# Kernel tuning notes

Hardware: AMD Instinct MI355X
Metric: run time of the kernel (lower is better)

The kernel has to match this reference:

```python
import jax, jax.numpy as jnp
import numpy as np

INNER_DIM = 1024

def setup_inputs() -> dict:
    key = jax.random.key(0)
    ks = jax.random.split(key, 6)
    b, n, d = 4, 4096, 1024
    s = 0.02
    return {
        "x": jax.random.normal(ks[0], (b, n, d), jnp.float32),
        "y": jax.random.normal(ks[1], (b, n, d), jnp.float32),
        "Wq": jax.random.normal(ks[2], (INNER_DIM, d), jnp.float32) * s,
        "Wk": jax.random.normal(ks[3], (INNER_DIM, d), jnp.float32) * s,
        "Wv": jax.random.normal(ks[4], (INNER_DIM, d), jnp.float32) * s,
        "Wo": jax.random.normal(ks[5], (d, INNER_DIM), jnp.float32) * s,
        "bo": jnp.zeros((d,), jnp.float32),
    }

def reference(x, y, Wq, Wk, Wv, Wo, bo):
    # torch Linear: out = inp @ W.T ; weights stored [out_dim, in_dim]
    q = jnp.einsum('bnd,ed->bne', y, Wq)  # queries come from y
    k = jnp.einsum('bnd,ed->bne', x, Wk)
    v = jnp.einsum('bnd,ed->bne', x, Wv)
    dk = 1.0 / jnp.sqrt(jnp.asarray(INNER_DIM, q.dtype))  # full inner_dim, not per-head
    alpha = jnp.einsum('bie,bje->bij', q, k) * dk  # [b, n, n] full score matrix
    alpha = jax.nn.softmax(alpha, axis=-1)
    # NOTE: original masked_fill is a no-op (result discarded), so no causal mask.
    ctx = jnp.einsum('bij,bje->bie', alpha, v)
    return jnp.einsum('bie,de->bid', ctx, Wo) + bo
```

## Files before the change

kernel.cpp:

```cpp
#include <hip/hip_runtime.h>
#include <stdint.h>

typedef __attribute__((ext_vector_type(8))) short s16x8;
typedef __attribute__((ext_vector_type(4))) float f32x4;

__device__ __forceinline__ unsigned short f2bf(float f) {
    union { float f; uint32_t u; } c; c.f = f;
    uint32_t u = c.u + 0x7FFFu + ((c.u >> 16) & 1u);
    return (unsigned short)(u >> 16);
}

__device__ __forceinline__ float bf2f(unsigned int u16) {
    union { uint32_t u; float f; } c; c.u = u16 << 16;
    return c.f;
}

__device__ __forceinline__ void load_lds16(const unsigned short* g, unsigned short* l) {
    __builtin_amdgcn_global_load_lds(
        (const __attribute__((address_space(1))) char*)(uintptr_t)g,
        (__attribute__((address_space(3))) char*)(uint32_t)(uintptr_t)l,
        16, 0, 0);
}

__device__ __forceinline__ void gemm256_core(
    const unsigned short* __restrict__ Ap, long lda,
    const unsigned short* __restrict__ Bp, long ldb,
    int nt, unsigned short* As, unsigned short* Bs, f32x4 (*acc)[4])
{
    const int tid  = threadIdx.x;
    const int wv   = tid >> 6;
    const int lane = tid & 63;
    const int cl   = lane & 15;
    const int qd   = lane >> 4;
    const int wm   = wv >> 2;
    const int wn   = wv & 3;

    long srcA[2][2], srcB[2][2];
    int  dstL[2][2];
#pragma unroll
    for (int h = 0; h < 2; ++h) {
#pragma unroll
        for (int c = 0; c < 2; ++c) {
            const int q0    = (wv << 7) + (c << 6);
            const int phys0 = q0 + (q0 & 512) + (h << 9);
            const int phys  = phys0 + lane;
            const int g     = phys >> 3;
            const long koff = (long)(((lane & 7) ^ (g & 7)) << 3);
            srcA[h][c] = (long)g * lda + koff;
            srcB[h][c] = (long)g * ldb + koff;
            dstL[h][c] = phys0 << 3;
        }
    }

    const int k0off = (((qd    ) ^ (cl & 7)) << 3) + cl * 64;
    const int k1off = (((4 + qd) ^ (cl & 7)) << 3) + cl * 64;

    load_lds16(Bp + srcB[0][0], Bs + dstL[0][0]);
    load_lds16(Bp + srcB[0][1], Bs + dstL[0][1]);
    load_lds16(Bp + srcB[1][0], Bs + dstL[1][0]);
    load_lds16(Bp + srcB[1][1], Bs + dstL[1][1]);
    load_lds16(Ap + srcA[0][0], As + dstL[0][0]);
    load_lds16(Ap + srcA[0][1], As + dstL[0][1]);
    load_lds16(Ap + srcA[1][0], As + dstL[1][0]);
    load_lds16(Ap + srcA[1][1], As + dstL[1][1]);
    asm volatile("s_waitcnt vmcnt(2)" ::: "memory");
    asm volatile("s_barrier" ::: "memory");

    for (int t = 0; t < nt; ++t) {
        const unsigned short* Ab = As + ((t & 1) << 14);
        const unsigned short* Bb = Bs + ((t & 1) << 14);
        unsigned short* An = As + (((t + 1) & 1) << 14);
        unsigned short* Bn = Bs + (((t + 1) & 1) << 14);
        const long kn   = (long)(t + 1) << 6;
        const bool more = (t + 1) < nt;
        s16x8 bfr[4][2];
#pragma unroll
        for (int p = 0; p < 4; ++p) {
            s16x8 af[2][2];
#pragma unroll
            for (int i = 0; i < 2; ++i) {
                const int s = (wm << 3) + (p << 1) + i;
                af[i][0] = *(const s16x8*)&Ab[s * 1024 + k0off];
                af[i][1] = *(const s16x8*)&Ab[s * 1024 + k1off];
            }
            if (p == 0) {
#pragma unroll
                for (int j = 0; j < 4; ++j) {
                    const int s = (wn << 2) + j;
                    bfr[j][0] = *(const s16x8*)&Bb[s * 1024 + k0off];
                    bfr[j][1] = *(const s16x8*)&Bb[s * 1024 + k1off];
                }
            }
            if (more) {
                if (p == 0)      { load_lds16(Bp + kn + srcB[0][0], Bn + dstL[0][0]);
                                   load_lds16(Bp + kn + srcB[0][1], Bn + dstL[0][1]); }
                else if (p == 1) { load_lds16(Bp + kn + srcB[1][0], Bn + dstL[1][0]);
                                   load_lds16(Bp + kn + srcB[1][1], Bn + dstL[1][1]); }
                else if (p == 2) { load_lds16(Ap + kn + srcA[0][0], An + dstL[0][0]);
                                   load_lds16(Ap + kn + srcA[0][1], An + dstL[0][1]); }
                else             { load_lds16(Ap + kn + srcA[1][0], An + dstL[1][0]);
                                   load_lds16(Ap + kn + srcA[1][1], An + dstL[1][1]); }
            }
            __builtin_amdgcn_s_setprio(1);
#pragma unroll
            for (int i = 0; i < 2; ++i)
#pragma unroll
                for (int j = 0; j < 4; ++j) {
                    acc[p * 2 + i][j] = __builtin_amdgcn_mfma_f32_16x16x32_bf16(
                        af[i][0], bfr[j][0], acc[p * 2 + i][j], 0, 0, 0);
                    acc[p * 2 + i][j] = __builtin_amdgcn_mfma_f32_16x16x32_bf16(
                        af[i][1], bfr[j][1], acc[p * 2 + i][j], 0, 0, 0);
                }
            __builtin_amdgcn_s_setprio(0);
            if (p == 1) {
                if (more) asm volatile("s_waitcnt vmcnt(4)" ::: "memory");
                else      asm volatile("s_waitcnt vmcnt(0)" ::: "memory");
            } else if (p == 3) {
                if (more) asm volatile("s_waitcnt vmcnt(2)" ::: "memory");
            }
            asm volatile("s_barrier" ::: "memory");
        }
    }
}

template <bool OUT_BF16, bool HAS_BIAS, bool EXP_OUT>
__global__ __launch_bounds__(512, 2)
void gemm256(const unsigned short* __restrict__ A, long lda, long sA,
             const unsigned short* __restrict__ B, long ldb, long sB,
             void* __restrict__ C, long ldc, long sC,
             const float* __restrict__ bias, int K, float scale)
{
    __shared__ __align__(16) unsigned short As[2 * 16384];
    __shared__ __align__(16) unsigned short Bs[2 * 16384];

    const unsigned gx = gridDim.x, gy = gridDim.y;
    const unsigned lin = blockIdx.x + gx * blockIdx.y;
    unsigned bxs, bys;
    if ((gy & 7u) == 0u) {
        const unsigned g = lin & 7u, j = lin >> 3;
        bxs = j & (gx - 1u);
        bys = g * (gy >> 3) + j / gx;
    } else { bxs = blockIdx.x; bys = blockIdx.y; }

    const unsigned short* Ap = A + (long)blockIdx.z * sA + (long)bys * 256 * lda;
    const unsigned short* Bp = B + (long)blockIdx.z * sB + (long)bxs * 256 * ldb;

    f32x4 acc[8][4];
#pragma unroll
    for (int i = 0; i < 8; ++i)
#pragma unroll
        for (int j = 0; j < 4; ++j)
            acc[i][j] = f32x4{0.f, 0.f, 0.f, 0.f};

    gemm256_core(Ap, lda, Bp, ldb, K >> 6, As, Bs, acc);

    const int wv = threadIdx.x >> 6;
    const int wm = wv >> 2, wn = wv & 3;
    const int cl = threadIdx.x & 15, qd = (threadIdx.x & 63) >> 4;
    const long row0 = (long)bys * 256 + wm * 128;
    const long col0 = (long)bxs * 256 + wn * 64;
    const long zC   = (long)blockIdx.z * sC;
#pragma unroll
    for (int j = 0; j < 4; ++j) {
        const long c = col0 + j * 16 + cl;
        float badd = 0.f;
        if constexpr (HAS_BIAS) badd = bias[c];
#pragma unroll
        for (int i = 0; i < 8; ++i) {
            const long rb = row0 + i * 16 + qd * 4;
#pragma unroll
            for (int r = 0; r < 4; ++r) {
                float v = acc[i][j][r] * scale + badd;
                if constexpr (EXP_OUT) v = __expf(v);
                const long idx = zC + (rb + r) * ldc + c;
                if constexpr (OUT_BF16) ((unsigned short*)C)[idx] = f2bf(v);
                else                    ((float*)C)[idx] = v;
            }
        }
    }
}

__global__ __launch_bounds__(512, 2)
void gemm256_pv4(const unsigned short* __restrict__ p0,
                 const unsigned short* __restrict__ p1,
                 const unsigned short* __restrict__ p2,
                 const unsigned short* __restrict__ p3,
                 const unsigned short* __restrict__ Bv, long ldb, long sB,
                 unsigned short* __restrict__ C, long ldc, long sC,
                 const float* __restrict__ rowdiv, int K, long lda)
{
    __shared__ __align__(16) unsigned short As[2 * 16384];
    __shared__ __align__(16) unsigned short Bs[2 * 16384];

    const unsigned gx = gridDim.x, gy = gridDim.y;
    const unsigned lin = blockIdx.x + gx * blockIdx.y;
    unsigned bxs, bys;
    if ((gy & 7u) == 0u) {
        const unsigned g = lin & 7u, j = lin >> 3;
        bxs = j & (gx - 1u);
        bys = g * (gy >> 3) + j / gx;
    } else { bxs = blockIdx.x; bys = blockIdx.y; }

    const int z = blockIdx.z;
    const unsigned short* A = (z == 0) ? p0 : (z == 1) ? p1 : (z == 2) ? p2 : p3;

    const unsigned short* Ap = A + (long)bys * 256 * lda;
    const unsigned short* Bp = Bv + (long)z * sB + (long)bxs * 256 * ldb;

    f32x4 acc[8][4];
#pragma unroll
    for (int i = 0; i < 8; ++i)
#pragma unroll
        for (int j = 0; j < 4; ++j)
            acc[i][j] = f32x4{0.f, 0.f, 0.f, 0.f};

    gemm256_core(Ap, lda, Bp, ldb, K >> 6, As, Bs, acc);

    const int wv = threadIdx.x >> 6;
    const int wm = wv >> 2, wn = wv & 3;
    const int cl = threadIdx.x & 15, qd = (threadIdx.x & 63) >> 4;
    const long row0 = (long)bys * 256 + wm * 128;
    const long col0 = (long)bxs * 256 + wn * 64;
    const long zC   = (long)z * sC;
    const float* rd = rowdiv + (long)z * 4096;
#pragma unroll
    for (int i = 0; i < 8; ++i) {
        const long rb = row0 + i * 16 + qd * 4;
        float rinv[4];
#pragma unroll
        for (int r = 0; r < 4; ++r) rinv[r] = 1.f / rd[rb + r];
#pragma unroll
        for (int j = 0; j < 4; ++j) {
            const long c = col0 + j * 16 + cl;
#pragma unroll
            for (int r = 0; r < 4; ++r)
                C[zC + (rb + r) * ldc + c] = f2bf(acc[i][j][r] * rinv[r]);
        }
    }
}

__global__ __launch_bounds__(256)
void rowsum4(const unsigned short* __restrict__ p0,
             const unsigned short* __restrict__ p1,
             const unsigned short* __restrict__ p2,
             const unsigned short* __restrict__ p3,
             float* __restrict__ rs)
{
    const unsigned row = blockIdx.x;
    const unsigned b = row >> 12;
    const unsigned short* P = (b == 0) ? p0 : (b == 1) ? p1 : (b == 2) ? p2 : p3;
    const long r = row & 4095u;
    const int tid = threadIdx.x, lane = tid & 63, wave = tid >> 6;

    const uint4* src = (const uint4*)(P + r * 4096);
    uint4 u0 = src[tid], u1 = src[tid + 256];
    float s = 0.f;
    {
        const unsigned* a = (const unsigned*)&u0;
        const unsigned* c = (const unsigned*)&u1;
#pragma unroll
        for (int i = 0; i < 4; ++i) {
            s += bf2f(a[i] & 0xFFFFu) + bf2f(a[i] >> 16);
            s += bf2f(c[i] & 0xFFFFu) + bf2f(c[i] >> 16);
        }
    }
#pragma unroll
    for (int off = 32; off > 0; off >>= 1) s += __shfl_xor(s, off);
    __shared__ float red[4];
    if (lane == 0) red[wave] = s;
    __syncthreads();
    if (tid == 0) rs[row] = red[0] + red[1] + red[2] + red[3];
}

__global__ __launch_bounds__(256)
void cast2_bf16(const float* __restrict__ s0, unsigned short* __restrict__ d0,
                const float* __restrict__ s1, unsigned short* __restrict__ d1)
{
    const float*    in  = blockIdx.y ? s1 : s0;
    unsigned short* out = blockIdx.y ? d1 : d0;
    const long i = ((long)blockIdx.x * 256 + threadIdx.x) * 4;
    const float4 v = *(const float4*)(in + i);
    ushort4 o;
    o.x = f2bf(v.x); o.y = f2bf(v.y); o.z = f2bf(v.z); o.w = f2bf(v.w);
    *(ushort4*)(out + i) = o;
}

__global__ __launch_bounds__(256)
void cast4_bf16(const float* __restrict__ s0, unsigned short* __restrict__ d0,
                const float* __restrict__ s1, unsigned short* __restrict__ d1,
                const float* __restrict__ s2, unsigned short* __restrict__ d2,
                const float* __restrict__ s3, unsigned short* __restrict__ d3)
{
    const float* in; unsigned short* out;
    switch (blockIdx.y) {
        case 0: in = s0; out = d0; break;
        case 1: in = s1; out = d1; break;
        case 2: in = s2; out = d2; break;
        default: in = s3; out = d3; break;
    }
    const long i = ((long)blockIdx.x * 256 + threadIdx.x) * 4;
    const float4 v = *(const float4*)(in + i);
    ushort4 o;
    o.x = f2bf(v.x); o.y = f2bf(v.y); o.z = f2bf(v.z); o.w = f2bf(v.w);
    *(ushort4*)(out + i) = o;
}

extern "C" void kernel_launch(void* const* d_in, const int* in_sizes, int n_in,
                              void* d_out, int out_size, void* d_ws, size_t ws_size,
                              hipStream_t stream)
{
    (void)in_sizes; (void)n_in; (void)out_size;
    const float* x  = (const float*)d_in[0];
    const float* y  = (const float*)d_in[1];
    const float* Wq = (const float*)d_in[2];
    const float* Wk = (const float*)d_in[3];
    const float* Wv = (const float*)d_in[4];
    const float* Wo = (const float*)d_in[5];
    const float* bo = (const float*)d_in[6];
    float* out = (float*)d_out;

    const long N = 4096, D = 1024;
    const long NB = N * D;
    const size_t MiB = 1ull << 20;
    const float dk = 0.03125f;
    char* w = (char*)d_ws;

    if (ws_size >= 200 * MiB) {
        unsigned short* Xb  = (unsigned short*)(w);
        unsigned short* Yb  = (unsigned short*)(w + 32 * MiB);
        unsigned short* Qb  = (unsigned short*)(w + 64 * MiB);
        unsigned short* Kb  = (unsigned short*)(w + 96 * MiB);
        unsigned short* VT  = (unsigned short*)(w + 128 * MiB);
        unsigned short* Wqb = (unsigned short*)(w + 192 * MiB);
        unsigned short* Wkb = (unsigned short*)(w + 194 * MiB);
        unsigned short* Wvb = (unsigned short*)(w + 196 * MiB);
        unsigned short* Wob = (unsigned short*)(w + 198 * MiB);
        unsigned short* P0  = (unsigned short*)(w);
        unsigned short* P1  = (unsigned short*)(w + 32 * MiB);
        unsigned short* P2  = (unsigned short*)(w + 160 * MiB);
        unsigned short* P3  = (unsigned short*)d_out;
        unsigned short* Cx  = (unsigned short*)(w + 64 * MiB);
        float*          rsm = (float*)(w + 192 * MiB);

        cast2_bf16<<<dim3(16384, 2), dim3(256), 0, stream>>>(x, Xb, y, Yb);
        cast4_bf16<<<dim3(1024, 4),  dim3(256), 0, stream>>>(
            Wq, Wqb, Wk, Wkb, Wv, Wvb, Wo, Wob);

        gemm256<true, false, false><<<dim3(4, 64, 2), dim3(512), 0, stream>>>(
            Yb, D, (long)(Xb - Yb), Wqb, D, (long)(Wkb - Wqb),
            Qb, D, (long)(Kb - Qb), nullptr, (int)D, 1.f);
        gemm256<true, false, false><<<dim3(16, 4, 4), dim3(512), 0, stream>>>(
            Wvb, D, 0, Xb, D, NB, VT, N, NB, nullptr, (int)D, 1.f);

        gemm256<true, false, true><<<dim3(16, 16, 2), dim3(512), 0, stream>>>(
            Qb, D, NB, Kb, D, NB, P0, N, (long)(P1 - P0), nullptr, (int)D, dk);
        gemm256<true, false, true><<<dim3(16, 16, 2), dim3(512), 0, stream>>>(
            Qb + 2 * NB, D, NB, Kb + 2 * NB, D, NB,
            P2, N, (long)(P3 - P2), nullptr, (int)D, dk);
        rowsum4<<<dim3(16384), dim3(256), 0, stream>>>(P0, P1, P2, P3, rsm);

        gemm256_pv4<<<dim3(4, 16, 4), dim3(512), 0, stream>>>(
            P0, P1, P2, P3, VT, N, NB, Cx, D, NB, rsm, (int)N, N);
        gemm256<false, true, false><<<dim3(4, 64, 1), dim3(512), 0, stream>>>(
            Cx, D, 0, Wob, D, 0, out, D, 0, bo, (int)D, 1.f);
    } else if (ws_size >= 104 * MiB) {
        unsigned short* Wqb = (unsigned short*)(w);
        unsigned short* Wkb = (unsigned short*)(w + 2 * MiB);
        unsigned short* Wvb = (unsigned short*)(w + 4 * MiB);
        unsigned short* Wob = (unsigned short*)(w + 6 * MiB);
        unsigned short* xb  = (unsigned short*)(w + 8 * MiB);
        unsigned short* yb  = (unsigned short*)(w + 16 * MiB);
        unsigned short* Qb  = (unsigned short*)(w + 24 * MiB);
        unsigned short* Kb  = (unsigned short*)(w + 32 * MiB);
        unsigned short* VTb = (unsigned short*)(w + 40 * MiB);
        unsigned short* Cxb = (unsigned short*)(w + 48 * MiB);
        unsigned short* Pb  = (unsigned short*)(w + 56 * MiB);
        float*          rsm = (float*)(w + 88 * MiB);

        cast4_bf16<<<dim3(1024, 4), dim3(256), 0, stream>>>(
            Wq, Wqb, Wk, Wkb, Wv, Wvb, Wo, Wob);

        for (int b = 0; b < 4; ++b) {
            cast2_bf16<<<dim3(4096, 2), dim3(256), 0, stream>>>(
                x + b * NB, xb, y + b * NB, yb);
            gemm256<true, false, false><<<dim3(4, 16, 1), dim3(512), 0, stream>>>(
                yb, D, 0, Wqb, D, 0, Qb, D, 0, nullptr, (int)D, 1.f);
            gemm256<true, false, false><<<dim3(4, 16, 1), dim3(512), 0, stream>>>(
                xb, D, 0, Wkb, D, 0, Kb, D, 0, nullptr, (int)D, 1.f);
            gemm256<true, false, false><<<dim3(16, 4, 1), dim3(512), 0, stream>>>(
                Wvb, D, 0, xb, D, 0, VTb, N, 0, nullptr, (int)D, 1.f);
            gemm256<true, false, true><<<dim3(16, 16, 1), dim3(512), 0, stream>>>(
                Qb, D, 0, Kb, D, 0, Pb, N, 0, nullptr, (int)D, dk);
            rowsum4<<<dim3(4096), dim3(256), 0, stream>>>(Pb, Pb, Pb, Pb, rsm);
            gemm256_pv4<<<dim3(4, 16, 1), dim3(512), 0, stream>>>(
                Pb, Pb, Pb, Pb, VTb, N, 0, Cxb, D, 0, rsm, (int)N, N);
            gemm256<false, true, false><<<dim3(4, 16, 1), dim3(512), 0, stream>>>(
                Cxb, D, 0, Wob, D, 0, out + b * NB, D, 0, bo, (int)D, 1.f);
        }
    }
}
```

Before: 640.0 us.

## Deepen GEMM K-loop pipeline to prefetch two tiles ahead with unrolled phases

Restructures the 256x256 GEMM core so global-to-LDS loads are issued roughly a full K-tile further ahead. The loop is unrolled by two over the double-buffered LDS, with eight phases per iteration and explicit vmcnt waits. Each phase now places barriers both before and after its MFMA block. The aim is to hide global load latency behind more MFMA work. In exchange it doubles the number of barriers, assumes nt is even, and relies on hand-tuned waitcnt values for correctness.

```diff
diff --git a/kernel.cpp b/kernel.cpp
--- a/kernel.cpp
+++ b/kernel.cpp
@@ -38,7 +38,7 @@
     long srcA[2][2], srcB[2][2];
     int  dstL[2][2];
 #pragma unroll
-    for (int h = 0; h < 2; ++h) {
+    for (int h = 0; h < 2; ++h)
 #pragma unroll
         for (int c = 0; c < 2; ++c) {
             const int q0    = (wv << 7) + (c << 6);
@@ -50,77 +50,95 @@
             srcB[h][c] = (long)g * ldb + koff;
             dstL[h][c] = phys0 << 3;
         }
-    }
 
     const int k0off = (((qd    ) ^ (cl & 7)) << 3) + cl * 64;
     const int k1off = (((4 + qd) ^ (cl & 7)) << 3) + cl * 64;
-
-    load_lds16(Bp + srcB[0][0], Bs + dstL[0][0]);
-    load_lds16(Bp + srcB[0][1], Bs + dstL[0][1]);
-    load_lds16(Bp + srcB[1][0], Bs + dstL[1][0]);
-    load_lds16(Bp + srcB[1][1], Bs + dstL[1][1]);
-    load_lds16(Ap + srcA[0][0], As + dstL[0][0]);
-    load_lds16(Ap + srcA[0][1], As + dstL[0][1]);
-    load_lds16(Ap + srcA[1][0], As + dstL[1][0]);
-    load_lds16(Ap + srcA[1][1], As + dstL[1][1]);
-    asm volatile("s_waitcnt vmcnt(2)" ::: "memory");
-    asm volatile("s_barrier" ::: "memory");
-
-    for (int t = 0; t < nt; ++t) {
-        const unsigned short* Ab = As + ((t & 1) << 14);
-        const unsigned short* Bb = Bs + ((t & 1) << 14);
-        unsigned short* An = As + (((t + 1) & 1) << 14);
-        unsigned short* Bn = Bs + (((t + 1) & 1) << 14);
-        const long kn   = (long)(t + 1) << 6;
-        const bool more = (t + 1) < nt;
-        s16x8 bfr[4][2];
-#pragma unroll
-        for (int p = 0; p < 4; ++p) {
-            s16x8 af[2][2];
-#pragma unroll
-            for (int i = 0; i < 2; ++i) {
-                const int s = (wm << 3) + (p << 1) + i;
-                af[i][0] = *(const s16x8*)&Ab[s * 1024 + k0off];
-                af[i][1] = *(const s16x8*)&Ab[s * 1024 + k1off];
-            }
-            if (p == 0) {
-#pragma unroll
-                for (int j = 0; j < 4; ++j) {
-                    const int s = (wn << 2) + j;
-                    bfr[j][0] = *(const s16x8*)&Bb[s * 1024 + k0off];
-                    bfr[j][1] = *(const s16x8*)&Bb[s * 1024 + k1off];
-                }
-            }
-            if (more) {
-                if (p == 0)      { load_lds16(Bp + kn + srcB[0][0], Bn + dstL[0][0]);
-                                   load_lds16(Bp + kn + srcB[0][1], Bn + dstL[0][1]); }
-                else if (p == 1) { load_lds16(Bp + kn + srcB[1][0], Bn + dstL[1][0]);
-                                   load_lds16(Bp + kn + srcB[1][1], Bn + dstL[1][1]); }
-                else if (p == 2) { load_lds16(Ap + kn + srcA[0][0], An + dstL[0][0]);
-                                   load_lds16(Ap + kn + srcA[0][1], An + dstL[0][1]); }
-                else             { load_lds16(Ap + kn + srcA[1][0], An + dstL[1][0]);
-                                   load_lds16(Ap + kn + srcA[1][1], An + dstL[1][1]); }
-            }
-            __builtin_amdgcn_s_setprio(1);
-#pragma unroll
-            for (int i = 0; i < 2; ++i)
-#pragma unroll
-                for (int j = 0; j < 4; ++j) {
-                    acc[p * 2 + i][j] = __builtin_amdgcn_mfma_f32_16x16x32_bf16(
-                        af[i][0], bfr[j][0], acc[p * 2 + i][j], 0, 0, 0);
-                    acc[p * 2 + i][j] = __builtin_amdgcn_mfma_f32_16x16x32_bf16(
-                        af[i][1], bfr[j][1], acc[p * 2 + i][j], 0, 0, 0);
-                }
-            __builtin_amdgcn_s_setprio(0);
-            if (p == 1) {
-                if (more) asm volatile("s_waitcnt vmcnt(4)" ::: "memory");
-                else      asm volatile("s_waitcnt vmcnt(0)" ::: "memory");
-            } else if (p == 3) {
-                if (more) asm volatile("s_waitcnt vmcnt(2)" ::: "memory");
-            }
-            asm volatile("s_barrier" ::: "memory");
-        }
-    }
+    const int aB = wm << 3;
+    const int bB = wn << 2;
+
+#define STAGE_A(buf, kb, h) do {                                             \
+        load_lds16(Ap + (kb) + srcA[h][0], As + ((buf) << 14) + dstL[h][0]); \
+        load_lds16(Ap + (kb) + srcA[h][1], As + ((buf) << 14) + dstL[h][1]); \
+    } while (0)
+#define STAGE_B(buf, kb, h) do {                                             \
+        load_lds16(Bp + (kb) + srcB[h][0], Bs + ((buf) << 14) + dstL[h][0]); \
+        load_lds16(Bp + (kb) + srcB[h][1], Bs + ((buf) << 14) + dstL[h][1]); \
+    } while (0)
+#define VMW(n) asm volatile("s_waitcnt vmcnt(" #n ")" ::: "memory")
+#define BAR()  asm volatile("s_barrier" ::: "memory")
+
+    STAGE_B(0, 0, 0); STAGE_B(0, 0, 1); STAGE_A(0, 0, 0); STAGE_A(0, 0, 1);
+    STAGE_B(1, 64, 0); STAGE_B(1, 64, 1); STAGE_A(1, 64, 0);
+    VMW(8);
+    BAR();
+
+    s16x8 bfr[4][2];
+
+#define PHASE(AB, BB, Q, RB, STG, WT) do {                                   \
+        const unsigned short* Ab_ = As + ((AB) << 14);                       \
+        const unsigned short* Bb_ = Bs + ((BB) << 14);                       \
+        s16x8 af_[2][2];                                                     \
+        _Pragma("unroll")                                                    \
+        for (int i_ = 0; i_ < 2; ++i_) {                                     \
+            const int s_ = aB + (Q) * 2 + i_;                                \
+            af_[i_][0] = *(const s16x8*)&Ab_[s_ * 1024 + k0off];             \
+            af_[i_][1] = *(const s16x8*)&Ab_[s_ * 1024 + k1off];             \
+        }                                                                    \
+        if (RB) {                                                            \
+            _Pragma("unroll")                                                \
+            for (int j_ = 0; j_ < 4; ++j_) {                                 \
+                const int s_ = bB + j_;                                      \
+                bfr[j_][0] = *(const s16x8*)&Bb_[s_ * 1024 + k0off];         \
+                bfr[j_][1] = *(const s16x8*)&Bb_[s_ * 1024 + k1off];         \
+            }                                                                \
+        }                                                                    \
+        STG;                                                                 \
+        WT;                                                                  \
+        BAR();                                                               \
+        __builtin_amdgcn_s_setprio(1);                                       \
+        _Pragma("unroll")                                                    \
+        for (int i_ = 0; i_ < 2; ++i_)                                       \
+            _Pragma("unroll")                                                \
+            for (int j_ = 0; j_ < 4; ++j_) {                                 \
+                acc[(Q) * 2 + i_][j_] =                                      \
+                    __builtin_amdgcn_mfma_f32_16x16x32_bf16(                 \
+                        af_[i_][0], bfr[j_][0], acc[(Q) * 2 + i_][j_],       \
+                        0, 0, 0);                                            \
+                acc[(Q) * 2 + i_][j_] =                                      \
+                    __builtin_amdgcn_mfma_f32_16x16x32_bf16(                 \
+                        af_[i_][1], bfr[j_][1], acc[(Q) * 2 + i_][j_],       \
+                        0, 0, 0);                                            \
+            }                                                                \
+        __builtin_amdgcn_s_setprio(0);                                       \
+        BAR();                                                               \
+    } while (0)
+
+    const int ni = nt >> 1;
+#pragma unroll 1
+    for (int it = 0; it < ni; ++it) {
+        const bool more = (it + 1) < ni;
+        const long kb_o  = ((long)(2 * it + 1)) << 6;
+        const long kb_e2 = ((long)(2 * it + 2)) << 6;
+        const long kb_o2 = ((long)(2 * it + 3)) << 6;
+
+        PHASE(0, 0, 0, true,  STAGE_A(1, kb_o, 1), (void)0);
+        PHASE(0, 0, 1, false, if (more) STAGE_B(0, kb_e2, 0),
+              if (more) VMW(10); else VMW(8));
+        PHASE(0, 0, 2, false, if (more) STAGE_B(0, kb_e2, 1), (void)0);
+        PHASE(0, 0, 3, false, if (more) STAGE_A(0, kb_e2, 0),
+              if (more) VMW(8); else VMW(2));
+        PHASE(1, 1, 0, true,  if (more) STAGE_A(0, kb_e2, 1), (void)0);
+        PHASE(1, 1, 1, false, if (more) STAGE_B(1, kb_o2, 0),
+              if (more) VMW(10); else VMW(0));
+        PHASE(1, 1, 2, false, if (more) STAGE_B(1, kb_o2, 1), (void)0);
+        PHASE(1, 1, 3, false, if (more) STAGE_A(1, kb_o2, 0),
+              if (more) VMW(8));
+    }
+#undef PHASE
+#undef STAGE_A
+#undef STAGE_B
+#undef VMW
+#undef BAR
 }
 
 template <bool OUT_BF16, bool HAS_BIAS, bool EXP_OUT>
```

After: 644.6 us. No clear change (+0.7%).
